# Performance work log

Hardware: AMD Instinct MI355X
Metric: run time of the kernel (lower is better)

## Reference

```python
import jax, jax.numpy as jnp
import numpy as np

N = 50000
NFEAT = 128
NHID = 64
EPS = 1e-5
NEG_SLOPE = 0.2


def gat_conv(x, src, dst, W, a_src, a_dst, b):
    # x: [N, in], W: [out, in], a_src/a_dst: [out], b: [out]
    h = x @ W.T                                   # [N, out]
    alpha_s = h @ a_src                           # [N]
    alpha_d = h @ a_dst                           # [N]
    e = jax.nn.leaky_relu(alpha_s[src] + alpha_d[dst], NEG_SLOPE)  # [E]
    # segment softmax over destination nodes
    m = jax.ops.segment_max(e, dst, num_segments=N)
    e = jnp.exp(e - m[dst])
    s = jax.ops.segment_sum(e, dst, num_segments=N)
    alpha = e / (s[dst] + 1e-16)
    out = jax.ops.segment_sum(alpha[:, None] * h[src], dst, num_segments=N)
    return out + b


def batch_norm(x, gamma, beta):
    mu = jnp.mean(x, axis=0)
    var = jnp.mean((x - mu) ** 2, axis=0)
    return gamma * (x - mu) * jax.lax.rsqrt(var + EPS) + beta


def setup_inputs() -> dict:
    key = jax.random.key(0)
    ks = jax.random.split(key, 24)
    E = 800000
    x = jax.random.normal(ks[0], (N, NFEAT), dtype=jnp.float32)
    edge_index = jax.random.randint(ks[1], (2, E), 0, N, dtype=jnp.int64)

    def lin(k, o, i):
        return jax.random.normal(k, (o, i), dtype=jnp.float32) / np.sqrt(i)

    def att(k, o):
        return jax.random.normal(k, (o,), dtype=jnp.float32) / np.sqrt(o)

    return dict(
        x=x, edge_index=edge_index,
        W1=lin(ks[2], NHID, NFEAT), a1s=att(ks[3], NHID), a1d=att(ks[4], NHID), b1=jnp.zeros((NHID,), jnp.float32),
        g1=jnp.ones((NHID,), jnp.float32), be1=jnp.zeros((NHID,), jnp.float32),
        W2=lin(ks[5], NHID, NHID), a2s=att(ks[6], NHID), a2d=att(ks[7], NHID), b2=jnp.zeros((NHID,), jnp.float32),
        g2=jnp.ones((NHID,), jnp.float32), be2=jnp.zeros((NHID,), jnp.float32),
        W3=lin(ks[8], NHID, NHID), a3s=att(ks[9], NHID), a3d=att(ks[10], NHID), b3=jnp.zeros((NHID,), jnp.float32),
        g3=jnp.ones((NHID,), jnp.float32), be3=jnp.zeros((NHID,), jnp.float32),
        W4=lin(ks[11], NFEAT, NHID), a4s=att(ks[12], NFEAT), a4d=att(ks[13], NFEAT), b4=jnp.zeros((NFEAT,), jnp.float32),
    )


def reference(x, edge_index, W1, a1s, a1d, b1, g1, be1, W2, a2s, a2d, b2, g2, be2,
              W3, a3s, a3d, b3, g3, be3, W4, a4s, a4d, b4):
    loops = jnp.arange(N, dtype=edge_index.dtype)
    src = jnp.concatenate([edge_index[0], loops])  # add self-loops (PyG default)
    dst = jnp.concatenate([edge_index[1], loops])
    # Encoder
    h = jax.nn.relu(gat_conv(x, src, dst, W1, a1s, a1d, b1))
    h = batch_norm(h, g1, be1)
    h = jax.nn.relu(gat_conv(h, src, dst, W2, a2s, a2d, b2))
    h = batch_norm(h, g2, be2)
    # Attribute decoder
    h = jax.nn.relu(gat_conv(h, src, dst, W3, a3s, a3d, b3))
    h = batch_norm(h, g3, be3)
    x_hat = jax.nn.relu(gat_conv(h, src, dst, W4, a4s, a4d, b4))
    diff = jnp.abs(x - x_hat)
    return diff, x_hat
```

## Files before the change

### kernel.cpp

```cpp
#include <hip/hip_runtime.h>
#include <math.h>

#define NND 50000
#define EPSB 1e-5f
#define SLOPE 0.2f
#define NB 256
#define SBLK 128
#define BRANGE 196

typedef float vfloat4 __attribute__((ext_vector_type(4)));

__device__ __forceinline__ float lrelu(float v) { return v > 0.f ? v : SLOPE * v; }

__device__ __forceinline__ ushort f2bf(float f) {
    unsigned u = __float_as_uint(f);
    unsigned r = (u + 0x7fffu + ((u >> 16) & 1u)) >> 16;
    return (ushort)r;
}

__device__ __forceinline__ void nt_store4(float4 v, float4* p) {
    vfloat4 t = {v.x, v.y, v.z, v.w};
    __builtin_nontemporal_store(t, (vfloat4*)p);
}

__device__ __forceinline__ void acc8(float* a, uint4 w, float e) {
    a[0] += e * __uint_as_float(w.x << 16);
    a[1] += e * __uint_as_float(w.x & 0xffff0000u);
    a[2] += e * __uint_as_float(w.y << 16);
    a[3] += e * __uint_as_float(w.y & 0xffff0000u);
    a[4] += e * __uint_as_float(w.z << 16);
    a[5] += e * __uint_as_float(w.z & 0xffff0000u);
    a[6] += e * __uint_as_float(w.w << 16);
    a[7] += e * __uint_as_float(w.w & 0xffff0000u);
}


__global__ __launch_bounds__(256) void countC_kernel(const int* __restrict__ ei, int E,
                                                     int* __restrict__ cnt, int* __restrict__ C) {
    __shared__ int lc[NB];
    const int tid = threadIdx.x;
    for (int i = tid; i < NB; i += 256) lc[i] = 0;
    __syncthreads();
    const int per = (E + SBLK - 1) / SBLK;
    const int beg = blockIdx.x * per;
    const int end = min(beg + per, E);
    for (int i = beg + tid; i < end; i += 256) {
        int d = __builtin_nontemporal_load(&ei[E + i]);
        atomicAdd(&cnt[d], 1);
        atomicAdd(&lc[d / BRANGE], 1);
    }
    __syncthreads();
    for (int i = tid; i < NB; i += 256) C[i * SBLK + blockIdx.x] = lc[i];
}

__global__ __launch_bounds__(1024) void scanC_kernel(int* __restrict__ C) {
    __shared__ int ps[1024];
    const int t = threadIdx.x;
    int v[NB * SBLK / 1024];
    int s = 0;
#pragma unroll
    for (int j = 0; j < NB * SBLK / 1024; j++) {
        v[j] = C[t * (NB * SBLK / 1024) + j];
        s += v[j];
    }
    ps[t] = s;
    __syncthreads();
    for (int off = 1; off < 1024; off <<= 1) {
        int x = (t >= off) ? ps[t - off] : 0;
        __syncthreads();
        ps[t] += x;
        __syncthreads();
    }
    int ex = ps[t] - s;
#pragma unroll
    for (int j = 0; j < NB * SBLK / 1024; j++) {
        int tmp = v[j];
        C[t * (NB * SBLK / 1024) + j] = ex;
        ex += tmp;
    }
}

__global__ __launch_bounds__(256) void scatter_pairs_kernel(const int* __restrict__ ei, int E,
                                                            const int* __restrict__ C,
                                                            unsigned long long* __restrict__ pairs) {
    __shared__ int woff[NB];
    const int tid = threadIdx.x;
    for (int i = tid; i < NB; i += 256) woff[i] = C[i * SBLK + blockIdx.x];
    __syncthreads();
    const int per = (E + SBLK - 1) / SBLK;
    const int beg = blockIdx.x * per;
    const int end = min(beg + per, E);
    for (int i = beg + tid; i < end; i += 256) {
        int s = __builtin_nontemporal_load(&ei[i]);
        int d = __builtin_nontemporal_load(&ei[E + i]);
        int p = atomicAdd(&woff[d / BRANGE], 1);
        pairs[p] = ((unsigned long long)(unsigned)d << 32) | (unsigned)s;
    }
}

__global__ void scan1_kernel(const int* __restrict__ in, int n, int* __restrict__ outex,
                             int* __restrict__ bsum) {
    __shared__ int tmp[256];
    int tid = threadIdx.x;
    int i = blockIdx.x * 256 + tid;
    int v = (i < n) ? in[i] + 1 : 0;
    tmp[tid] = v;
    __syncthreads();
    for (int off = 1; off < 256; off <<= 1) {
        int t = (tid >= off) ? tmp[tid - off] : 0;
        __syncthreads();
        tmp[tid] += t;
        __syncthreads();
    }
    if (i < n) outex[i] = tmp[tid] - v;
    if (tid == 255) bsum[blockIdx.x] = tmp[255];
}

__global__ void scan2_kernel(const int* __restrict__ in, int n, int* __restrict__ outex) {
    __shared__ int tmp[256];
    int tid = threadIdx.x;
    int v = (tid < n) ? in[tid] : 0;
    tmp[tid] = v;
    __syncthreads();
    for (int off = 1; off < 256; off <<= 1) {
        int t = (tid >= off) ? tmp[tid - off] : 0;
        __syncthreads();
        tmp[tid] += t;
        __syncthreads();
    }
    if (tid < n) outex[tid] = tmp[tid] - v;
}

__global__ void scan3_kernel(int* __restrict__ rp, const int* __restrict__ boff,
                             int* __restrict__ fill, int* __restrict__ srcs, int n, int etot) {
    int i = blockIdx.x * 256 + threadIdx.x;
    if (i < n) {
        int v = rp[i] + boff[blockIdx.x];
        rp[i] = v;
        srcs[v] = i;
        fill[i] = v + 1;
    }
    if (i == 0) rp[n] = etot;
}

__global__ __launch_bounds__(256) void bucket_csr_kernel(const unsigned long long* __restrict__ pairs,
                                                         int E, const int* __restrict__ C,
                                                         int* __restrict__ fill,
                                                         int* __restrict__ srcs) {
    const int b = blockIdx.x;
    const int beg = C[b * SBLK];
    const int end = (b == NB - 1) ? E : C[(b + 1) * SBLK];
    for (int i = beg + threadIdx.x; i < end; i += 256) {
        unsigned long long pr = __builtin_nontemporal_load(&pairs[i]);
        int d = (int)(pr >> 32);
        int s = (int)(pr & 0xffffffffu);
        int p = atomicAdd(&fill[d], 1);
        srcs[p] = s;
    }
}


template <int K, int FOUT>
__global__ __launch_bounds__(256) void gemm_kernel(
    const float* __restrict__ X, const float* __restrict__ W, ushort* __restrict__ H, int n,
    const float* __restrict__ bnsum, const float* __restrict__ bnsq, const float* __restrict__ g,
    const float* __restrict__ be, const float* __restrict__ asrc, const float* __restrict__ adst,
    float* __restrict__ as_o, float* __restrict__ ad_o) {
    constexpr int SW = FOUT + 4;
    constexpr int SX = 68;
    constexpr int NF = FOUT / 64;
    __shared__ float Wt[64 * SW];
    __shared__ float Xt[64 * SX];
    __shared__ float bnsc[K];
    __shared__ float bnsh[K];
    const int tid = threadIdx.x;
    const int nodeBase = blockIdx.x * 64;
    const int tx = tid & 15, ty = tid >> 4;
    const bool doBN = (bnsum != nullptr);

    if (doBN) {
        const float invn = 1.f / (float)NND;
        for (int f = tid; f < K; f += 256) {
            float mu = bnsum[f] * invn;
            float var = bnsq[f] * invn - mu * mu;
            float r = rsqrtf(var + EPSB);
            float sc = g[f] * r;
            bnsc[f] = sc;
            bnsh[f] = be[f] - mu * sc;
        }
    }
    __syncthreads();

    float acc[4][4 * NF];
#pragma unroll
    for (int i = 0; i < 4; i++)
#pragma unroll
        for (int j = 0; j < 4 * NF; j++) acc[i][j] = 0.f;

    for (int kc = 0; kc < K; kc += 64) {
        for (int idx = tid; idx < FOUT * 64; idx += 256) {
            int f = idx >> 6, kk = idx & 63;
            Wt[kk * SW + f] = W[f * K + kc + kk];
        }
        for (int idx = tid; idx < 64 * 16; idx += 256) {
            int r = idx >> 4, c4 = idx & 15;
            int node = nodeBase + r;
            float4 v = make_float4(0.f, 0.f, 0.f, 0.f);
            if (node < n) {
                v = ((const float4*)X)[node * (K / 4) + (kc >> 2) + c4];
                if (doBN) {
                    int f = kc + c4 * 4;
                    v.x = v.x * bnsc[f + 0] + bnsh[f + 0];
                    v.y = v.y * bnsc[f + 1] + bnsh[f + 1];
                    v.z = v.z * bnsc[f + 2] + bnsh[f + 2];
                    v.w = v.w * bnsc[f + 3] + bnsh[f + 3];
                }
            }
            Xt[(c4 * 4 + 0) * SX + r] = v.x;
            Xt[(c4 * 4 + 1) * SX + r] = v.y;
            Xt[(c4 * 4 + 2) * SX + r] = v.z;
            Xt[(c4 * 4 + 3) * SX + r] = v.w;
        }
        __syncthreads();
#pragma unroll 16
        for (int k = 0; k < 64; k++) {
            const float4 xv = *(const float4*)(Xt + k * SX + ty * 4);
            const float4 wv = *(const float4*)(Wt + k * SW + tx * 4);
            const float xa[4] = {xv.x, xv.y, xv.z, xv.w};
            float wa[4 * NF];
            wa[0] = wv.x; wa[1] = wv.y; wa[2] = wv.z; wa[3] = wv.w;
            if constexpr (NF == 2) {
                const float4 wv2 = *(const float4*)(Wt + k * SW + 64 + tx * 4);
                wa[4] = wv2.x; wa[5] = wv2.y; wa[6] = wv2.z; wa[7] = wv2.w;
            }
#pragma unroll
            for (int i = 0; i < 4; i++)
#pragma unroll
                for (int j = 0; j < 4 * NF; j++) acc[i][j] += xa[i] * wa[j];
        }
        __syncthreads();
    }
#pragma unroll
    for (int i = 0; i < 4; i++) {
        int node = nodeBase + ty * 4 + i;
        if (node < n) {
            ushort4 o;
            o.x = f2bf(acc[i][0]); o.y = f2bf(acc[i][1]);
            o.z = f2bf(acc[i][2]); o.w = f2bf(acc[i][3]);
            ((ushort4*)H)[node * (FOUT / 4) + tx] = o;
            if constexpr (NF == 2) {
                ushort4 o2;
                o2.x = f2bf(acc[i][4]); o2.y = f2bf(acc[i][5]);
                o2.z = f2bf(acc[i][6]); o2.w = f2bf(acc[i][7]);
                ((ushort4*)H)[node * (FOUT / 4) + 16 + tx] = o2;
            }
        }
    }
    if (as_o) {
        float asv[4 * NF], adv[4 * NF];
#pragma unroll
        for (int j = 0; j < 4; j++) {
            asv[j] = asrc[tx * 4 + j];
            adv[j] = adst[tx * 4 + j];
            if constexpr (NF == 2) {
                asv[4 + j] = asrc[64 + tx * 4 + j];
                adv[4 + j] = adst[64 + tx * 4 + j];
            }
        }
#pragma unroll
        for (int i = 0; i < 4; i++) {
            int node = nodeBase + ty * 4 + i;
            float ps = 0.f, pd = 0.f;
#pragma unroll
            for (int j = 0; j < 4 * NF; j++) {
                ps += acc[i][j] * asv[j];
                pd += acc[i][j] * adv[j];
            }
#pragma unroll
            for (int off = 1; off < 16; off <<= 1) {
                ps += __shfl_xor(ps, off, 64);
                pd += __shfl_xor(pd, off, 64);
            }
            if (tx == 0 && node < n) {
                as_o[node] = ps;
                ad_o[node] = pd;
            }
        }
    }
}


template <int F, bool FINAL>
__global__ __launch_bounds__(256) void edge_kernel(
    const int* __restrict__ rp, const int* __restrict__ srcs, const float* __restrict__ as_,
    const float* __restrict__ ad_, const ushort* __restrict__ h, const float* __restrict__ bias,
    float* __restrict__ y, float* __restrict__ bnsum, float* __restrict__ bnsq,
    const float* __restrict__ xin, float* __restrict__ odiff, float* __restrict__ oxhat) {
    constexpr int GS = F / 8;
    constexpr int GPW = 64 / GS;
    const int tid = threadIdx.x;
    const int lane = tid & 63;
    const int wslot = tid >> 6;
    const int sub = lane & (GS - 1);
    const int grp = (blockIdx.x * 4 + wslot) * GPW + lane / GS;
    const int ngrp = gridDim.x * 4 * GPW;
    const float4 bA = ((const float4*)bias)[sub * 2];
    const float4 bB = ((const float4*)bias)[sub * 2 + 1];
    float st[8], qt[8];
#pragma unroll
    for (int j = 0; j < 8; j++) st[j] = qt[j] = 0.f;

    for (int row = grp; row < NND; row += ngrp) {
        const int beg = rp[row], end = rp[row + 1];
        const float ad = ad_[row];
        float a[8];
#pragma unroll
        for (int j = 0; j < 8; j++) a[j] = 0.f;
        float sw = 0.f;
        int i = beg;
        for (; i + 4 <= end; i += 4) {
            int s0 = __builtin_nontemporal_load(&srcs[i]);
            int s1 = __builtin_nontemporal_load(&srcs[i + 1]);
            int s2 = __builtin_nontemporal_load(&srcs[i + 2]);
            int s3 = __builtin_nontemporal_load(&srcs[i + 3]);
            uint4 h0 = *(const uint4*)(h + (size_t)s0 * F + sub * 8);
            uint4 h1 = *(const uint4*)(h + (size_t)s1 * F + sub * 8);
            uint4 h2 = *(const uint4*)(h + (size_t)s2 * F + sub * 8);
            uint4 h3 = *(const uint4*)(h + (size_t)s3 * F + sub * 8);
            float e0 = __expf(fminf(lrelu(as_[s0] + ad), 80.f));
            float e1 = __expf(fminf(lrelu(as_[s1] + ad), 80.f));
            float e2 = __expf(fminf(lrelu(as_[s2] + ad), 80.f));
            float e3 = __expf(fminf(lrelu(as_[s3] + ad), 80.f));
            acc8(a, h0, e0);
            acc8(a, h1, e1);
            acc8(a, h2, e2);
            acc8(a, h3, e3);
            sw += (e0 + e1) + (e2 + e3);
        }
        for (; i < end; i++) {
            int s0 = __builtin_nontemporal_load(&srcs[i]);
            uint4 h0 = *(const uint4*)(h + (size_t)s0 * F + sub * 8);
            float e0 = __expf(fminf(lrelu(as_[s0] + ad), 80.f));
            acc8(a, h0, e0);
            sw += e0;
        }
        const float inv = 1.f / (sw + 1e-16f);
        float4 ya, yb;
        ya.x = fmaxf(a[0] * inv + bA.x, 0.f);
        ya.y = fmaxf(a[1] * inv + bA.y, 0.f);
        ya.z = fmaxf(a[2] * inv + bA.z, 0.f);
        ya.w = fmaxf(a[3] * inv + bA.w, 0.f);
        yb.x = fmaxf(a[4] * inv + bB.x, 0.f);
        yb.y = fmaxf(a[5] * inv + bB.y, 0.f);
        yb.z = fmaxf(a[6] * inv + bB.z, 0.f);
        yb.w = fmaxf(a[7] * inv + bB.w, 0.f);
        if constexpr (FINAL) {
            const float4* xr = (const float4*)(xin + (size_t)row * F);
            float4 xa = xr[sub * 2], xb = xr[sub * 2 + 1];
            float4* xo = (float4*)(oxhat + (size_t)row * F);
            nt_store4(ya, &xo[sub * 2]);
            nt_store4(yb, &xo[sub * 2 + 1]);
            float4 da, db;
            da.x = fabsf(xa.x - ya.x); da.y = fabsf(xa.y - ya.y);
            da.z = fabsf(xa.z - ya.z); da.w = fabsf(xa.w - ya.w);
            db.x = fabsf(xb.x - yb.x); db.y = fabsf(xb.y - yb.y);
            db.z = fabsf(xb.z - yb.z); db.w = fabsf(xb.w - yb.w);
            float4* dio = (float4*)(odiff + (size_t)row * F);
            nt_store4(da, &dio[sub * 2]);
            nt_store4(db, &dio[sub * 2 + 1]);
        } else {
            float4* yo = (float4*)(y + (size_t)row * F);
            nt_store4(ya, &yo[sub * 2]);
            nt_store4(yb, &yo[sub * 2 + 1]);
            st[0] += ya.x; qt[0] += ya.x * ya.x;
            st[1] += ya.y; qt[1] += ya.y * ya.y;
            st[2] += ya.z; qt[2] += ya.z * ya.z;
            st[3] += ya.w; qt[3] += ya.w * ya.w;
            st[4] += yb.x; qt[4] += yb.x * yb.x;
            st[5] += yb.y; qt[5] += yb.y * yb.y;
            st[6] += yb.z; qt[6] += yb.z * yb.z;
            st[7] += yb.w; qt[7] += yb.w * yb.w;
        }
    }
    if constexpr (!FINAL) {
        __shared__ float redS[256][8];
        __shared__ float redQ[256][8];
#pragma unroll
        for (int j = 0; j < 8; j++) {
            redS[tid][j] = st[j];
            redQ[tid][j] = qt[j];
        }
        __syncthreads();
        if (tid < F) {
            int sb = tid >> 3, j = tid & 7;
            float ts = 0.f, tq = 0.f;
            for (int k = 0; k < 256 / GS; k++) {
                int t2 = k * GS + sb;
                ts += redS[t2][j];
                tq += redQ[t2][j];
            }
            atomicAdd(&bnsum[tid], ts);
            atomicAdd(&bnsq[tid], tq);
        }
    }
}


extern "C" void kernel_launch(void* const* d_in, const int* in_sizes, int n_in, void* d_out,
                              int out_size, void* d_ws, size_t ws_size, hipStream_t stream) {
    const float* x = (const float*)d_in[0];
    const int* ei = (const int*)d_in[1];
    const int E = in_sizes[1] / 2;
    const float* W1 = (const float*)d_in[2];
    const float* a1s = (const float*)d_in[3];
    const float* a1d = (const float*)d_in[4];
    const float* b1 = (const float*)d_in[5];
    const float* g1 = (const float*)d_in[6];
    const float* be1 = (const float*)d_in[7];
    const float* W2 = (const float*)d_in[8];
    const float* a2s = (const float*)d_in[9];
    const float* a2d = (const float*)d_in[10];
    const float* b2 = (const float*)d_in[11];
    const float* g2 = (const float*)d_in[12];
    const float* be2 = (const float*)d_in[13];
    const float* W3 = (const float*)d_in[14];
    const float* a3s = (const float*)d_in[15];
    const float* a3d = (const float*)d_in[16];
    const float* b3 = (const float*)d_in[17];
    const float* g3 = (const float*)d_in[18];
    const float* be3 = (const float*)d_in[19];
    const float* W4 = (const float*)d_in[20];
    const float* a4s = (const float*)d_in[21];
    const float* a4d = (const float*)d_in[22];
    const float* b4 = (const float*)d_in[23];

    const int Etot = E + NND;

    char* w = (char*)d_ws;
    auto alloc = [&](size_t bytes) {
        void* p = (void*)w;
        w += (bytes + 255) & ~(size_t)255;
        return p;
    };
    int* cnt = (int*)alloc((size_t)NND * 4);
    float* stats = (float*)alloc(384 * 4);
    int* rp = (int*)alloc((size_t)(NND + 1) * 4);
    int* fill = (int*)alloc((size_t)NND * 4);
    int* bsum = (int*)alloc(256 * 4);
    int* bsum2 = (int*)alloc(256 * 4);
    int* C = (int*)alloc((size_t)NB * SBLK * 4);
    unsigned long long* pairs = (unsigned long long*)alloc((size_t)E * 8);
    int* srcs = (int*)alloc((size_t)Etot * 4);
    ushort* bufH = (ushort*)alloc((size_t)NND * 128 * 2);
    float* bufY = (float*)alloc((size_t)NND * 64 * 4);
    float* asb = (float*)alloc((size_t)NND * 4);
    float* adb = (float*)alloc((size_t)NND * 4);

    const int nblk = (NND + 255) / 256;
    const int ggrid = (NND + 63) / 64;
    const int xgrid = 2048;

    hipError_t _e = hipMemsetAsync(cnt, 0, (((size_t)NND * 4 + 255) & ~(size_t)255) + 384 * 4, stream);
    (void)_e;

    countC_kernel<<<SBLK, 256, 0, stream>>>(ei, E, cnt, C);
    scan1_kernel<<<nblk, 256, 0, stream>>>(cnt, NND, rp, bsum);
    scan2_kernel<<<1, 256, 0, stream>>>(bsum, nblk, bsum2);
    scan3_kernel<<<nblk, 256, 0, stream>>>(rp, bsum2, fill, srcs, NND, Etot);
    scanC_kernel<<<1, 1024, 0, stream>>>(C);
    scatter_pairs_kernel<<<SBLK, 256, 0, stream>>>(ei, E, C, pairs);
    bucket_csr_kernel<<<NB, 256, 0, stream>>>(pairs, E, C, fill, srcs);

    gemm_kernel<128, 64><<<ggrid, 256, 0, stream>>>(x, W1, bufH, NND, nullptr, nullptr, nullptr,
                                                    nullptr, a1s, a1d, asb, adb);
    edge_kernel<64, false><<<xgrid, 256, 0, stream>>>(rp, srcs, asb, adb, bufH, b1, bufY,
                                                      stats + 0, stats + 64, nullptr, nullptr,
                                                      nullptr);
    gemm_kernel<64, 64><<<ggrid, 256, 0, stream>>>(bufY, W2, bufH, NND, stats + 0, stats + 64,
                                                   g1, be1, a2s, a2d, asb, adb);
    edge_kernel<64, false><<<xgrid, 256, 0, stream>>>(rp, srcs, asb, adb, bufH, b2, bufY,
                                                      stats + 128, stats + 192, nullptr, nullptr,
                                                      nullptr);
    gemm_kernel<64, 64><<<ggrid, 256, 0, stream>>>(bufY, W3, bufH, NND, stats + 128, stats + 192,
                                                   g2, be2, a3s, a3d, asb, adb);
    edge_kernel<64, false><<<xgrid, 256, 0, stream>>>(rp, srcs, asb, adb, bufH, b3, bufY,
                                                      stats + 256, stats + 320, nullptr, nullptr,
                                                      nullptr);
    float* odiff = (float*)d_out;
    float* oxhat = (float*)d_out + (size_t)NND * 128;
    gemm_kernel<64, 128><<<ggrid, 256, 0, stream>>>(bufY, W4, bufH, NND, stats + 256, stats + 320,
                                                    g3, be3, a4s, a4d, asb, adb);
    edge_kernel<128, true><<<xgrid, 256, 0, stream>>>(rp, srcs, asb, adb, bufH, b4, nullptr,
                                                      nullptr, nullptr, x, odiff, oxhat);
}
```

Measured before the change: 547.6 us.

## Use atomic work-stealing row scheduling in edge kernels, drop nontemporal hints

Edge kernels now fetch batches of destination rows per wavefront from a global atomic counter instead of a static grid-stride assignment, and the grid shrinks from 2048 to 1024 blocks. This targets load imbalance from variable node degrees. Nontemporal loads and stores are replaced with ordinary ones, and the memset is extended to zero the per-layer counters. The cost is one atomic per wavefront per batch of rows, and the changed cache behaviour for the srcs and output streams.

```diff
diff --git a/kernel.cpp b/kernel.cpp
--- a/kernel.cpp
+++ b/kernel.cpp
@@ -8,19 +8,12 @@
 #define SBLK 128
 #define BRANGE 196
 
-typedef float vfloat4 __attribute__((ext_vector_type(4)));
-
 __device__ __forceinline__ float lrelu(float v) { return v > 0.f ? v : SLOPE * v; }
 
 __device__ __forceinline__ ushort f2bf(float f) {
     unsigned u = __float_as_uint(f);
     unsigned r = (u + 0x7fffu + ((u >> 16) & 1u)) >> 16;
     return (ushort)r;
-}
-
-__device__ __forceinline__ void nt_store4(float4 v, float4* p) {
-    vfloat4 t = {v.x, v.y, v.z, v.w};
-    __builtin_nontemporal_store(t, (vfloat4*)p);
 }
 
 __device__ __forceinline__ void acc8(float* a, uint4 w, float e) {
@@ -295,91 +288,94 @@
     const int* __restrict__ rp, const int* __restrict__ srcs, const float* __restrict__ as_,
     const float* __restrict__ ad_, const ushort* __restrict__ h, const float* __restrict__ bias,
     float* __restrict__ y, float* __restrict__ bnsum, float* __restrict__ bnsq,
-    const float* __restrict__ xin, float* __restrict__ odiff, float* __restrict__ oxhat) {
+    const float* __restrict__ xin, float* __restrict__ odiff, float* __restrict__ oxhat,
+    int* __restrict__ ctr) {
     constexpr int GS = F / 8;
     constexpr int GPW = 64 / GS;
     const int tid = threadIdx.x;
     const int lane = tid & 63;
-    const int wslot = tid >> 6;
     const int sub = lane & (GS - 1);
-    const int grp = (blockIdx.x * 4 + wslot) * GPW + lane / GS;
-    const int ngrp = gridDim.x * 4 * GPW;
+    const int gInW = lane / GS;
     const float4 bA = ((const float4*)bias)[sub * 2];
     const float4 bB = ((const float4*)bias)[sub * 2 + 1];
     float st[8], qt[8];
 #pragma unroll
     for (int j = 0; j < 8; j++) st[j] = qt[j] = 0.f;
 
-    for (int row = grp; row < NND; row += ngrp) {
-        const int beg = rp[row], end = rp[row + 1];
-        const float ad = ad_[row];
-        float a[8];
-#pragma unroll
-        for (int j = 0; j < 8; j++) a[j] = 0.f;
-        float sw = 0.f;
-        int i = beg;
-        for (; i + 4 <= end; i += 4) {
-            int s0 = __builtin_nontemporal_load(&srcs[i]);
-            int s1 = __builtin_nontemporal_load(&srcs[i + 1]);
-            int s2 = __builtin_nontemporal_load(&srcs[i + 2]);
-            int s3 = __builtin_nontemporal_load(&srcs[i + 3]);
-            uint4 h0 = *(const uint4*)(h + (size_t)s0 * F + sub * 8);
-            uint4 h1 = *(const uint4*)(h + (size_t)s1 * F + sub * 8);
-            uint4 h2 = *(const uint4*)(h + (size_t)s2 * F + sub * 8);
-            uint4 h3 = *(const uint4*)(h + (size_t)s3 * F + sub * 8);
-            float e0 = __expf(fminf(lrelu(as_[s0] + ad), 80.f));
-            float e1 = __expf(fminf(lrelu(as_[s1] + ad), 80.f));
-            float e2 = __expf(fminf(lrelu(as_[s2] + ad), 80.f));
-            float e3 = __expf(fminf(lrelu(as_[s3] + ad), 80.f));
-            acc8(a, h0, e0);
-            acc8(a, h1, e1);
-            acc8(a, h2, e2);
-            acc8(a, h3, e3);
-            sw += (e0 + e1) + (e2 + e3);
-        }
-        for (; i < end; i++) {
-            int s0 = __builtin_nontemporal_load(&srcs[i]);
-            uint4 h0 = *(const uint4*)(h + (size_t)s0 * F + sub * 8);
-            float e0 = __expf(fminf(lrelu(as_[s0] + ad), 80.f));
-            acc8(a, h0, e0);
-            sw += e0;
-        }
-        const float inv = 1.f / (sw + 1e-16f);
-        float4 ya, yb;
-        ya.x = fmaxf(a[0] * inv + bA.x, 0.f);
-        ya.y = fmaxf(a[1] * inv + bA.y, 0.f);
-        ya.z = fmaxf(a[2] * inv + bA.z, 0.f);
-        ya.w = fmaxf(a[3] * inv + bA.w, 0.f);
-        yb.x = fmaxf(a[4] * inv + bB.x, 0.f);
-        yb.y = fmaxf(a[5] * inv + bB.y, 0.f);
-        yb.z = fmaxf(a[6] * inv + bB.z, 0.f);
-        yb.w = fmaxf(a[7] * inv + bB.w, 0.f);
-        if constexpr (FINAL) {
-            const float4* xr = (const float4*)(xin + (size_t)row * F);
-            float4 xa = xr[sub * 2], xb = xr[sub * 2 + 1];
-            float4* xo = (float4*)(oxhat + (size_t)row * F);
-            nt_store4(ya, &xo[sub * 2]);
-            nt_store4(yb, &xo[sub * 2 + 1]);
-            float4 da, db;
-            da.x = fabsf(xa.x - ya.x); da.y = fabsf(xa.y - ya.y);
-            da.z = fabsf(xa.z - ya.z); da.w = fabsf(xa.w - ya.w);
-            db.x = fabsf(xb.x - yb.x); db.y = fabsf(xb.y - yb.y);
-            db.z = fabsf(xb.z - yb.z); db.w = fabsf(xb.w - yb.w);
-            float4* dio = (float4*)(odiff + (size_t)row * F);
-            nt_store4(da, &dio[sub * 2]);
-            nt_store4(db, &dio[sub * 2 + 1]);
-        } else {
-            float4* yo = (float4*)(y + (size_t)row * F);
-            nt_store4(ya, &yo[sub * 2]);
-            nt_store4(yb, &yo[sub * 2 + 1]);
-            st[0] += ya.x; qt[0] += ya.x * ya.x;
-            st[1] += ya.y; qt[1] += ya.y * ya.y;
-            st[2] += ya.z; qt[2] += ya.z * ya.z;
-            st[3] += ya.w; qt[3] += ya.w * ya.w;
-            st[4] += yb.x; qt[4] += yb.x * yb.x;
-            st[5] += yb.y; qt[5] += yb.y * yb.y;
-            st[6] += yb.z; qt[6] += yb.z * yb.z;
-            st[7] += yb.w; qt[7] += yb.w * yb.w;
+    for (;;) {
+        int base = 0;
+        if (lane == 0) base = atomicAdd(ctr, GPW);
+        base = __shfl(base, 0, 64);
+        if (base >= NND) break;
+        const int row = base + gInW;
+        if (row < NND) {
+            const int beg = rp[row], end = rp[row + 1];
+            const float ad = ad_[row];
+            float a[8];
+#pragma unroll
+            for (int j = 0; j < 8; j++) a[j] = 0.f;
+            float sw = 0.f;
+            int i = beg;
+            for (; i + 4 <= end; i += 4) {
+                int s0 = srcs[i], s1 = srcs[i + 1], s2 = srcs[i + 2], s3 = srcs[i + 3];
+                uint4 h0 = *(const uint4*)(h + (size_t)s0 * F + sub * 8);
+                uint4 h1 = *(const uint4*)(h + (size_t)s1 * F + sub * 8);
+                uint4 h2 = *(const uint4*)(h + (size_t)s2 * F + sub * 8);
+                uint4 h3 = *(const uint4*)(h + (size_t)s3 * F + sub * 8);
+                float e0 = __expf(fminf(lrelu(as_[s0] + ad), 80.f));
+                float e1 = __expf(fminf(lrelu(as_[s1] + ad), 80.f));
+                float e2 = __expf(fminf(lrelu(as_[s2] + ad), 80.f));
+                float e3 = __expf(fminf(lrelu(as_[s3] + ad), 80.f));
+                acc8(a, h0, e0);
+                acc8(a, h1, e1);
+                acc8(a, h2, e2);
+                acc8(a, h3, e3);
+                sw += (e0 + e1) + (e2 + e3);
+            }
+            for (; i < end; i++) {
+                int s0 = srcs[i];
+                uint4 h0 = *(const uint4*)(h + (size_t)s0 * F + sub * 8);
+                float e0 = __expf(fminf(lrelu(as_[s0] + ad), 80.f));
+                acc8(a, h0, e0);
+                sw += e0;
+            }
+            const float inv = 1.f / (sw + 1e-16f);
+            float4 ya, yb;
+            ya.x = fmaxf(a[0] * inv + bA.x, 0.f);
+            ya.y = fmaxf(a[1] * inv + bA.y, 0.f);
+            ya.z = fmaxf(a[2] * inv + bA.z, 0.f);
+            ya.w = fmaxf(a[3] * inv + bA.w, 0.f);
+            yb.x = fmaxf(a[4] * inv + bB.x, 0.f);
+            yb.y = fmaxf(a[5] * inv + bB.y, 0.f);
+            yb.z = fmaxf(a[6] * inv + bB.z, 0.f);
+            yb.w = fmaxf(a[7] * inv + bB.w, 0.f);
+            if constexpr (FINAL) {
+                const float4* xr = (const float4*)(xin + (size_t)row * F);
+                float4 xa = xr[sub * 2], xb = xr[sub * 2 + 1];
+                float4* xo = (float4*)(oxhat + (size_t)row * F);
+                xo[sub * 2] = ya;
+                xo[sub * 2 + 1] = yb;
+                float4 da, db;
+                da.x = fabsf(xa.x - ya.x); da.y = fabsf(xa.y - ya.y);
+                da.z = fabsf(xa.z - ya.z); da.w = fabsf(xa.w - ya.w);
+                db.x = fabsf(xb.x - yb.x); db.y = fabsf(xb.y - yb.y);
+                db.z = fabsf(xb.z - yb.z); db.w = fabsf(xb.w - yb.w);
+                float4* dio = (float4*)(odiff + (size_t)row * F);
+                dio[sub * 2] = da;
+                dio[sub * 2 + 1] = db;
+            } else {
+                float4* yo = (float4*)(y + (size_t)row * F);
+                yo[sub * 2] = ya;
+                yo[sub * 2 + 1] = yb;
+                st[0] += ya.x; qt[0] += ya.x * ya.x;
+                st[1] += ya.y; qt[1] += ya.y * ya.y;
+                st[2] += ya.z; qt[2] += ya.z * ya.z;
+                st[3] += ya.w; qt[3] += ya.w * ya.w;
+                st[4] += yb.x; qt[4] += yb.x * yb.x;
+                st[5] += yb.y; qt[5] += yb.y * yb.y;
+                st[6] += yb.z; qt[6] += yb.z * yb.z;
+                st[7] += yb.w; qt[7] += yb.w * yb.w;
+            }
         }
     }
     if constexpr (!FINAL) {
@@ -444,6 +440,7 @@
     };
     int* cnt = (int*)alloc((size_t)NND * 4);
     float* stats = (float*)alloc(384 * 4);
+    int* rowctr = (int*)alloc(4 * 4);
     int* rp = (int*)alloc((size_t)(NND + 1) * 4);
     int* fill = (int*)alloc((size_t)NND * 4);
     int* bsum = (int*)alloc(256 * 4);
@@ -458,9 +455,10 @@
 
     const int nblk = (NND + 255) / 256;
     const int ggrid = (NND + 63) / 64;
-    const int xgrid = 2048;
-
-    hipError_t _e = hipMemsetAsync(cnt, 0, (((size_t)NND * 4 + 255) & ~(size_t)255) + 384 * 4, stream);
+    const int xgrid = 1024;
+
+    const size_t msz = (((size_t)NND * 4 + 255) & ~(size_t)255) + ((384 * 4 + 255) & ~255) + 256;
+    hipError_t _e = hipMemsetAsync(cnt, 0, msz, stream);
     (void)_e;
 
     countC_kernel<<<SBLK, 256, 0, stream>>>(ei, E, cnt, C);
@@ -475,21 +473,22 @@
                                                     nullptr, a1s, a1d, asb, adb);
     edge_kernel<64, false><<<xgrid, 256, 0, stream>>>(rp, srcs, asb, adb, bufH, b1, bufY,
                                                       stats + 0, stats + 64, nullptr, nullptr,
-                                                      nullptr);
+                                                      nullptr, rowctr + 0);
     gemm_kernel<64, 64><<<ggrid, 256, 0, stream>>>(bufY, W2, bufH, NND, stats + 0, stats + 64,
                                                    g1, be1, a2s, a2d, asb, adb);
     edge_kernel<64, false><<<xgrid, 256, 0, stream>>>(rp, srcs, asb, adb, bufH, b2, bufY,
                                                       stats + 128, stats + 192, nullptr, nullptr,
-                                                      nullptr);
+                                                      nullptr, rowctr + 1);
     gemm_kernel<64, 64><<<ggrid, 256, 0, stream>>>(bufY, W3, bufH, NND, stats + 128, stats + 192,
                                                    g2, be2, a3s, a3d, asb, adb);
     edge_kernel<64, false><<<xgrid, 256, 0, stream>>>(rp, srcs, asb, adb, bufH, b3, bufY,
                                                       stats + 256, stats + 320, nullptr, nullptr,
-                                                      nullptr);
+                                                      nullptr, rowctr + 2);
     float* odiff = (float*)d_out;
     float* oxhat = (float*)d_out + (size_t)NND * 128;
     gemm_kernel<64, 128><<<ggrid, 256, 0, stream>>>(bufY, W4, bufH, NND, stats + 256, stats + 320,
                                                     g3, be3, a4s, a4d, asb, adb);
     edge_kernel<128, true><<<xgrid, 256, 0, stream>>>(rp, srcs, asb, adb, bufH, b4, nullptr,
-                                                      nullptr, nullptr, x, odiff, oxhat);
-}
+                                                      nullptr, nullptr, x, odiff, oxhat,
+                                                      rowctr + 3);
+}
```

New measurement: 884.1 us. +61.5%, slower.
